# Kernel optimization log

Measured on AMD Instinct MI355X. Metric: run time of the kernel, lower is better.

## Reference

```python
import jax, jax.numpy as jnp
import numpy as np

BS, T_SEG, C, D, N, K, H = 4, 16, 64, 64, 4096, 32, 64
STRIDE = 4
NB, BSZ, NG, BPG = 4, 8, 1, 4  # K = NB*BSZ, NB = NG*BPG (dendritic tree covers all K)
EPS = 1e-8


def _forward(cc_signals, h_prev, prev_messages, trace_prim, trace_key,
             primitives, key_p, decay_logit, dendrite_branch_w, dendrite_group_w,
             fc1_w, fc1_b, fc2_w, fc2_b, mod_lr_logit, conn_indices):
    bs, n, d = h_prev.shape
    # ---- per-neuron modulator MLP: [h, trace_prim, trace_key, primitives, key] -> 3 ----
    mod_input = jnp.concatenate([
        h_prev, trace_prim, trace_key,
        jnp.broadcast_to(primitives[None], (bs, n, d)),
        jnp.broadcast_to(key_p[None], (bs, n, d))], axis=-1)           # [BS,N,5D]
    x = jnp.tanh(jnp.einsum('bnd,ndh->bnh', mod_input, fc1_w) + fc1_b)  # [BS,N,H]
    out3 = jnp.einsum('bnh,nho->bno', x, fc2_w) + fc2_b                 # [BS,N,3]
    gate_prim = jnp.tanh(out3[..., 0:1])
    gate_key = jnp.tanh(out3[..., 1:2])
    decay_mod = out3[..., 2]

    mod_lr = jax.nn.sigmoid(mod_lr_logit)
    tp_dir = trace_prim / jnp.clip(jnp.linalg.norm(trace_prim, axis=-1, keepdims=True), EPS)
    tk_dir = trace_key / jnp.clip(jnp.linalg.norm(trace_key, axis=-1, keepdims=True), EPS)
    eff_prim = primitives[None] + mod_lr * gate_prim * tp_dir           # [BS,N,D]
    eff_key = key_p[None] + mod_lr * gate_key * tk_dir                  # [BS,N,D]
    eff_decay = jax.nn.sigmoid(decay_logit[None] + decay_mod)[..., None]  # [BS,N,1]

    # routing computed once per segment from the initial messages
    routing = jax.nn.sigmoid(
        jnp.einsum('bnd,bnkd->bnk', eff_key, prev_messages[:, conn_indices]))  # [BS,N,K]

    def gather_fc(weighted):  # [BS,N,K,D] -> [BS,N,D] hierarchical dendritic reduce
        tree = weighted.reshape(bs, n, NB, BSZ, d)
        branch = jnp.tanh(jnp.einsum('bnjkd,njkd->bnjd', tree, dendrite_branch_w))  # [BS,N,NB,D]
        grouped = branch.reshape(bs, n, NG, BPG, d)
        group = jnp.tanh(jnp.einsum('bngpd,ngpd->bngd', grouped, dendrite_group_w))  # [BS,N,NG,D]
        return group.mean(axis=2)  # n_tree == K so no leftover term

    cc_steps = jnp.moveaxis(cc_signals[:, ::STRIDE], 0, 1)  # [n_steps,BS,C,D]

    def step(carry, cc_t):
        h, prev_msg = carry
        nm = prev_msg[:, conn_indices]                      # neighbor gather [BS,N,K,D]
        received = gather_fc(routing[..., None] * nm)       # [BS,N,D]
        received = received.at[:, :C].add(cc_t)             # inject port signals
        h = eff_decay * h + (1.0 - eff_decay) * received
        prev_msg = jnp.tanh(h * eff_prim)
        return (h, prev_msg), prev_msg[:, :C]

    (h_final, _), ports = jax.lax.scan(step, (h_prev, prev_messages), cc_steps)
    # each port output is held for `stride` tokens; only the fresh one carries grad
    ports_rep = jnp.repeat(ports, STRIDE, axis=0)            # [T,BS,C,D]
    fresh = (jnp.arange(T_SEG) % STRIDE == 0)[:, None, None, None]
    out = jnp.where(fresh, ports_rep, jax.lax.stop_gradient(ports_rep))
    return jnp.moveaxis(out, 0, 1)                           # [BS,T_seg,C,D]


def setup_inputs() -> dict:
    key = jax.random.key(0)
    ks = jax.random.split(key, 10)

    def rms_init(k, shape):
        raw = jax.random.normal(k, shape, dtype=jnp.float32)
        rms = jnp.clip(jnp.sqrt(jnp.mean(raw ** 2, axis=-1, keepdims=True)), EPS)
        return raw / rms

    cc_signals = jax.random.normal(ks[0], (BS, T_SEG, C, D), dtype=jnp.float32)
    h_prev = 0.1 * jax.random.normal(ks[1], (BS, N, D), dtype=jnp.float32)
    primitives = rms_init(ks[2], (N, D))
    key_p = rms_init(ks[3], (N, D))
    prev_messages = jnp.tanh(h_prev * primitives[None])
    trace_prim = 0.1 * jax.random.normal(ks[4], (BS, N, D), dtype=jnp.float32)
    trace_key = 0.1 * jax.random.normal(ks[5], (BS, N, D), dtype=jnp.float32)
    decay_logit = jnp.zeros((N,), dtype=jnp.float32)
    dendrite_branch_w = jnp.full((N, NB, BSZ, D), 1.0 / BSZ, dtype=jnp.float32)
    dendrite_group_w = jnp.full((N, NG, BPG, D), 1.0 / BPG, dtype=jnp.float32)
    fc1_w = jax.random.normal(ks[6], (N, 5 * D, H), dtype=jnp.float32) * (2.0 / (5 * D + H)) ** 0.5
    fc1_b = jnp.zeros((N, H), dtype=jnp.float32)
    fc2_w = 0.02 * jax.random.normal(ks[7], (N, H, 3), dtype=jnp.float32)
    fc2_b = jnp.zeros((N, 3), dtype=jnp.float32)
    mod_lr_logit = jnp.float32(-2.0)
    conn_indices = jnp.sort(jax.random.randint(ks[8], (N, K), 0, N, dtype=jnp.int32), axis=-1)
    return dict(cc_signals=cc_signals, h_prev=h_prev, prev_messages=prev_messages,
                trace_prim=trace_prim, trace_key=trace_key, primitives=primitives,
                key_p=key_p, decay_logit=decay_logit,
                dendrite_branch_w=dendrite_branch_w, dendrite_group_w=dendrite_group_w,
                fc1_w=fc1_w, fc1_b=fc1_b, fc2_w=fc2_w, fc2_b=fc2_b,
                mod_lr_logit=mod_lr_logit, conn_indices=conn_indices)


def reference(cc_signals, h_prev, prev_messages, trace_prim, trace_key,
              primitives, key_p, decay_logit, dendrite_branch_w, dendrite_group_w,
              fc1_w, fc1_b, fc2_w, fc2_b, mod_lr_logit, conn_indices):
    return _forward(cc_signals, h_prev, prev_messages, trace_prim, trace_key,
                    primitives, key_p, decay_logit, dendrite_branch_w, dendrite_group_w,
                    fc1_w, fc1_b, fc2_w, fc2_b, mod_lr_logit, conn_indices)
```

## Files before the change

kernel.cpp:

```cpp
#include <hip/hip_runtime.h>
#include <math.h>

#define BS 4
#define TSEG 16
#define CC 64
#define DD 64
#define NN 4096
#define KK 32
#define HH 64
#define D5 320

__device__ __forceinline__ float sigm(float x){ return 1.0f/(1.0f+expf(-x)); }

__global__ __launch_bounds__(256) void k_pre(
    const float* __restrict__ h_prev,
    const float* __restrict__ pm0,
    const float* __restrict__ trp,
    const float* __restrict__ trk,
    const float* __restrict__ prim,
    const float* __restrict__ keyp,
    const float* __restrict__ dlog,
    const float* __restrict__ fc1w,
    const float* __restrict__ fc1b,
    const float* __restrict__ fc2w,
    const float* __restrict__ fc2b,
    const float* __restrict__ mll,
    const int*  __restrict__ conn,
    float* __restrict__ ws_h,
    float* __restrict__ ws_ep,
    float* __restrict__ ws_rt,
    float* __restrict__ ws_ed)
{
    __shared__ float mod2[4][D5][4];
    __shared__ int   cn_s[4][KK];
    const int wid  = threadIdx.x >> 6;
    const int lane = threadIdx.x & 63;
    const int n    = (blockIdx.x << 2) + wid;

    #pragma unroll
    for (int b = 0; b < BS; b++) {
        mod2[wid][lane      ][b] = h_prev[((size_t)b*NN + n)*DD + lane];
        mod2[wid][64  + lane][b] = trp  [((size_t)b*NN + n)*DD + lane];
        mod2[wid][128 + lane][b] = trk  [((size_t)b*NN + n)*DD + lane];
    }
    {
        const float pv = prim[(size_t)n*DD + lane];
        const float kv = keyp[(size_t)n*DD + lane];
        #pragma unroll
        for (int b = 0; b < BS; b++) {
            mod2[wid][192 + lane][b] = pv;
            mod2[wid][256 + lane][b] = kv;
        }
    }
    if (lane < KK) cn_s[wid][lane] = conn[(size_t)n*KK + lane];
    __syncthreads();

    float acc[4] = {0.f, 0.f, 0.f, 0.f};
    const float* wp = fc1w + (size_t)n * D5 * HH + lane;
    #pragma unroll 8
    for (int d = 0; d < D5; d++) {
        const float  w  = wp[(size_t)d * HH];
        const float4 mv = *(const float4*)(&mod2[wid][d][0]);
        acc[0] = fmaf(mv.x, w, acc[0]);
        acc[1] = fmaf(mv.y, w, acc[1]);
        acc[2] = fmaf(mv.z, w, acc[2]);
        acc[3] = fmaf(mv.w, w, acc[3]);
    }
    const float b1 = fc1b[(size_t)n*HH + lane];
    float x[4];
    #pragma unroll
    for (int b = 0; b < BS; b++) x[b] = tanhf(acc[b] + b1);

    const float f0 = fc2w[(size_t)n*HH*3 + lane*3 + 0];
    const float f1 = fc2w[(size_t)n*HH*3 + lane*3 + 1];
    const float f2 = fc2w[(size_t)n*HH*3 + lane*3 + 2];
    float po[4][3];
    #pragma unroll
    for (int b = 0; b < BS; b++) { po[b][0]=x[b]*f0; po[b][1]=x[b]*f1; po[b][2]=x[b]*f2; }
    #pragma unroll
    for (int m = 1; m < 64; m <<= 1) {
        #pragma unroll
        for (int b = 0; b < BS; b++) {
            #pragma unroll
            for (int o = 0; o < 3; o++) po[b][o] += __shfl_xor(po[b][o], m, 64);
        }
    }
    const float c0 = fc2b[(size_t)n*3+0];
    const float c1 = fc2b[(size_t)n*3+1];
    const float c2 = fc2b[(size_t)n*3+2];
    const float dl  = dlog[n];
    const float mlr = sigm(mll[0]);
    float gp[4], gk[4], ed[4];
    #pragma unroll
    for (int b = 0; b < BS; b++) {
        gp[b] = tanhf(po[b][0] + c0);
        gk[b] = tanhf(po[b][1] + c1);
        ed[b] = sigm(dl + po[b][2] + c2);
    }
    {
        const float edsel = (lane==0)?ed[0]:(lane==1)?ed[1]:(lane==2)?ed[2]:ed[3];
        if (lane < 4) ws_ed[(size_t)lane*NN + n] = edsel;
    }

    const int d = lane;
    const float4 hpv = *(const float4*)(&mod2[wid][d      ][0]);
    const float4 tpv = *(const float4*)(&mod2[wid][64  + d][0]);
    const float4 tkv = *(const float4*)(&mod2[wid][128 + d][0]);
    const float  pr  = mod2[wid][192 + d][0];
    const float  kp  = mod2[wid][256 + d][0];
    float hp[4] = {hpv.x, hpv.y, hpv.z, hpv.w};
    float tp[4] = {tpv.x, tpv.y, tpv.z, tpv.w};
    float tk[4] = {tkv.x, tkv.y, tkv.z, tkv.w};

    float s2[8];
    #pragma unroll
    for (int b = 0; b < BS; b++) { s2[b] = tp[b]*tp[b]; s2[4+b] = tk[b]*tk[b]; }
    #pragma unroll
    for (int m = 1; m < 64; m <<= 1) {
        #pragma unroll
        for (int i = 0; i < 8; i++) s2[i] += __shfl_xor(s2[i], m, 64);
    }
    float ep[4], ek[4];
    #pragma unroll
    for (int b = 0; b < BS; b++) {
        const float np = fmaxf(sqrtf(s2[b]),   1e-8f);
        const float nk = fmaxf(sqrtf(s2[4+b]), 1e-8f);
        ep[b] = pr + mlr*gp[b]*(tp[b]/np);
        ek[b] = kp + mlr*gk[b]*(tk[b]/nk);
    }
    #pragma unroll
    for (int b = 0; b < BS; b++) {
        ws_ep[((size_t)b*NN + n)*DD + d] = ep[b];
        ws_h [((size_t)b*NN + n)*DD + d] = hp[b];
    }
    #pragma unroll 4
    for (int k = 0; k < KK; k++) {
        const int cn = cn_s[wid][k];
        float rr[4];
        #pragma unroll
        for (int b = 0; b < BS; b++) rr[b] = ek[b]*pm0[((size_t)b*NN + cn)*DD + d];
        #pragma unroll
        for (int m = 1; m < 64; m <<= 1) {
            #pragma unroll
            for (int b = 0; b < BS; b++) rr[b] += __shfl_xor(rr[b], m, 64);
        }
        const float rsel = (lane==0)?rr[0]:(lane==1)?rr[1]:(lane==2)?rr[2]:rr[3];
        if (lane < 4) ws_rt[((size_t)lane*NN + n)*KK + k] = sigm(rsel);
    }
}

__global__ __launch_bounds__(256) void k_step(
    const float* __restrict__ pm_in,
    float* __restrict__ pm_out,
    float* __restrict__ ws_h,
    const float* __restrict__ ws_ep,
    const float* __restrict__ ws_rt,
    const float* __restrict__ ws_ed,
    const float* __restrict__ bw,
    const float* __restrict__ gw,
    const int*  __restrict__ conn,
    const float* __restrict__ cc,
    float* __restrict__ out,
    const int s)
{
    __shared__ float bw_s[2048];
    __shared__ float gw_s[256];
    __shared__ float rt_s[4][KK];
    __shared__ int   cn_s[KK];
    const int n   = blockIdx.x;
    const int tid = threadIdx.x;
    {
        const float4* src = (const float4*)(bw + (size_t)n*2048);
        float4* dst = (float4*)bw_s;
        dst[tid]       = src[tid];
        dst[tid + 256] = src[tid + 256];
        if (tid < 64) ((float4*)gw_s)[tid] = ((const float4*)(gw + (size_t)n*256))[tid];
        if (tid < KK) cn_s[tid] = conn[(size_t)n*KK + tid];
        if (tid < 128) rt_s[tid>>5][tid&31] =
            ws_rt[((size_t)(tid>>5)*NN + n)*KK + (tid & 31)];
    }
    __syncthreads();

    const int b = tid >> 6, d = tid & 63;
    const size_t bn = ((size_t)b*NN + n)*DD + d;

    float bs0=0.f, bs1=0.f, bs2=0.f, bs3=0.f;
    #pragma unroll
    for (int k = 0; k < KK; k++) {
        const int   cn = cn_s[k];
        const float nm = pm_in[((size_t)b*NN + cn)*DD + d];
        const float wg = rt_s[b][k] * nm;
        const float bv = bw_s[k*DD + d];
        if      (k <  8) bs0 = fmaf(wg, bv, bs0);
        else if (k < 16) bs1 = fmaf(wg, bv, bs1);
        else if (k < 24) bs2 = fmaf(wg, bv, bs2);
        else             bs3 = fmaf(wg, bv, bs3);
    }
    const float br0 = tanhf(bs0), br1 = tanhf(bs1), br2 = tanhf(bs2), br3 = tanhf(bs3);
    const float gs = br0*gw_s[d] + br1*gw_s[64+d] + br2*gw_s[128+d] + br3*gw_s[192+d];
    float recv = tanhf(gs);
    if (n < CC) recv += cc[(size_t)((b*TSEG + 4*s)*CC + n)*DD + d];

    const float edv = ws_ed[(size_t)b*NN + n];
    const float hn  = edv*ws_h[bn] + (1.0f - edv)*recv;
    ws_h[bn] = hn;
    const float pmv = tanhf(hn * ws_ep[bn]);
    pm_out[bn] = pmv;
    if (n < CC) {
        #pragma unroll
        for (int r = 0; r < 4; r++)
            out[(size_t)((b*TSEG + 4*s + r)*CC + n)*DD + d] = pmv;
    }
}

extern "C" void kernel_launch(void* const* d_in, const int* in_sizes, int n_in,
                              void* d_out, int out_size, void* d_ws, size_t ws_size,
                              hipStream_t stream) {
    const float* cc    = (const float*)d_in[0];
    const float* h_prev= (const float*)d_in[1];
    const float* pm0   = (const float*)d_in[2];
    const float* trp   = (const float*)d_in[3];
    const float* trk   = (const float*)d_in[4];
    const float* prim  = (const float*)d_in[5];
    const float* keyp  = (const float*)d_in[6];
    const float* dlog  = (const float*)d_in[7];
    const float* bw    = (const float*)d_in[8];
    const float* gw    = (const float*)d_in[9];
    const float* fc1w  = (const float*)d_in[10];
    const float* fc1b  = (const float*)d_in[11];
    const float* fc2w  = (const float*)d_in[12];
    const float* fc2b  = (const float*)d_in[13];
    const float* mll   = (const float*)d_in[14];
    const int*   conn  = (const int*)d_in[15];
    float* out = (float*)d_out;

    float* ws   = (float*)d_ws;
    const size_t BND = (size_t)BS*NN*DD;
    float* ws_h  = ws;
    float* ws_ep = ws + BND;
    float* msgA  = ws + 2*BND;
    float* msgB  = ws + 3*BND;
    float* ws_rt = ws + 4*BND;
    float* ws_ed = ws + 4*BND + (size_t)BS*NN*KK;

    k_pre<<<NN/4, 256, 0, stream>>>(h_prev, pm0, trp, trk, prim, keyp, dlog,
                                    fc1w, fc1b, fc2w, fc2b, mll, conn,
                                    ws_h, ws_ep, ws_rt, ws_ed);

    k_step<<<NN, 256, 0, stream>>>(pm0,  msgA, ws_h, ws_ep, ws_rt, ws_ed,
                                   bw, gw, conn, cc, out, 0);
    k_step<<<NN, 256, 0, stream>>>(msgA, msgB, ws_h, ws_ep, ws_rt, ws_ed,
                                   bw, gw, conn, cc, out, 1);
    k_step<<<NN, 256, 0, stream>>>(msgB, msgA, ws_h, ws_ep, ws_rt, ws_ed,
                                   bw, gw, conn, cc, out, 2);
    k_step<<<NN, 256, 0, stream>>>(msgA, msgB, ws_h, ws_ep, ws_rt, ws_ed,
                                   bw, gw, conn, cc, out, 3);
}
```

Before: 616.8 us.

## Vectorize fc1 and routing in k_pre; make k_step wave-per-neuron with float4 I/O

The fc1 matvec is restructured so each lane loads float4 weight rows and accumulates a 4x4 register tile of batch by hidden outputs. The 320-long input dimension is split across four lane groups, which are then combined with shuffles. The routing dot products and k_step's gather, dendrite and update path now use float4 accesses. k_step maps one wavefront per neuron and four neurons per block, so the block barrier goes away. The initial h copy to the workspace is dropped, and step 0 reads h_prev directly. In exchange there are more live registers and more LDS per block, and the code relies on wavefront-level ordering of LDS writes and reads with no barrier.

```diff
diff --git a/kernel.cpp b/kernel.cpp
--- a/kernel.cpp
+++ b/kernel.cpp
@@ -11,6 +11,9 @@
 #define D5 320
 
 __device__ __forceinline__ float sigm(float x){ return 1.0f/(1.0f+expf(-x)); }
+__device__ __forceinline__ float4 tanh4(float4 v){
+    return make_float4(tanhf(v.x), tanhf(v.y), tanhf(v.z), tanhf(v.w));
+}
 
 __global__ __launch_bounds__(256) void k_pre(
     const float* __restrict__ h_prev,
@@ -26,12 +29,12 @@
     const float* __restrict__ fc2b,
     const float* __restrict__ mll,
     const int*  __restrict__ conn,
-    float* __restrict__ ws_h,
     float* __restrict__ ws_ep,
     float* __restrict__ ws_rt,
     float* __restrict__ ws_ed)
 {
     __shared__ float mod2[4][D5][4];
+    __shared__ float ek_s[4][4][DD];
     __shared__ int   cn_s[4][KK];
     const int wid  = threadIdx.x >> 6;
     const int lane = threadIdx.x & 63;
@@ -53,37 +56,71 @@
         }
     }
     if (lane < KK) cn_s[wid][lane] = conn[(size_t)n*KK + lane];
-    __syncthreads();
-
-    float acc[4] = {0.f, 0.f, 0.f, 0.f};
-    const float* wp = fc1w + (size_t)n * D5 * HH + lane;
-    #pragma unroll 8
-    for (int d = 0; d < D5; d++) {
-        const float  w  = wp[(size_t)d * HH];
-        const float4 mv = *(const float4*)(&mod2[wid][d][0]);
-        acc[0] = fmaf(mv.x, w, acc[0]);
-        acc[1] = fmaf(mv.y, w, acc[1]);
-        acc[2] = fmaf(mv.z, w, acc[2]);
-        acc[3] = fmaf(mv.w, w, acc[3]);
-    }
-    const float b1 = fc1b[(size_t)n*HH + lane];
-    float x[4];
-    #pragma unroll
-    for (int b = 0; b < BS; b++) x[b] = tanhf(acc[b] + b1);
-
-    const float f0 = fc2w[(size_t)n*HH*3 + lane*3 + 0];
-    const float f1 = fc2w[(size_t)n*HH*3 + lane*3 + 1];
-    const float f2 = fc2w[(size_t)n*HH*3 + lane*3 + 2];
-    float po[4][3];
-    #pragma unroll
-    for (int b = 0; b < BS; b++) { po[b][0]=x[b]*f0; po[b][1]=x[b]*f1; po[b][2]=x[b]*f2; }
-    #pragma unroll
-    for (int m = 1; m < 64; m <<= 1) {
-        #pragma unroll
-        for (int b = 0; b < BS; b++) {
-            #pragma unroll
-            for (int o = 0; o < 3; o++) po[b][o] += __shfl_xor(po[b][o], m, 64);
-        }
+
+    const int g  = lane >> 4;
+    const int hq = lane & 15;
+    float acc[16];
+    #pragma unroll
+    for (int i = 0; i < 16; i++) acc[i] = 0.f;
+    const float* wp = fc1w + (size_t)n*D5*HH + (size_t)g*HH + 4*hq;
+    const float* mp = &mod2[wid][g][0];
+    #pragma unroll 4
+    for (int it = 0; it < 80; it++) {
+        const float4 w4 = *(const float4*)(wp + (size_t)it*256);
+        const float4 m4 = *(const float4*)(mp + it*16);
+        acc[ 0] = fmaf(m4.x, w4.x, acc[ 0]);
+        acc[ 1] = fmaf(m4.x, w4.y, acc[ 1]);
+        acc[ 2] = fmaf(m4.x, w4.z, acc[ 2]);
+        acc[ 3] = fmaf(m4.x, w4.w, acc[ 3]);
+        acc[ 4] = fmaf(m4.y, w4.x, acc[ 4]);
+        acc[ 5] = fmaf(m4.y, w4.y, acc[ 5]);
+        acc[ 6] = fmaf(m4.y, w4.z, acc[ 6]);
+        acc[ 7] = fmaf(m4.y, w4.w, acc[ 7]);
+        acc[ 8] = fmaf(m4.z, w4.x, acc[ 8]);
+        acc[ 9] = fmaf(m4.z, w4.y, acc[ 9]);
+        acc[10] = fmaf(m4.z, w4.z, acc[10]);
+        acc[11] = fmaf(m4.z, w4.w, acc[11]);
+        acc[12] = fmaf(m4.w, w4.x, acc[12]);
+        acc[13] = fmaf(m4.w, w4.y, acc[13]);
+        acc[14] = fmaf(m4.w, w4.z, acc[14]);
+        acc[15] = fmaf(m4.w, w4.w, acc[15]);
+    }
+    #pragma unroll
+    for (int i = 0; i < 16; i++) {
+        acc[i] += __shfl_xor(acc[i], 16, 64);
+        acc[i] += __shfl_xor(acc[i], 32, 64);
+    }
+    const float4 b1 = *(const float4*)(fc1b + (size_t)n*HH + 4*hq);
+    float x[16];
+    #pragma unroll
+    for (int b = 0; b < BS; b++) {
+        x[b*4+0] = tanhf(acc[b*4+0] + b1.x);
+        x[b*4+1] = tanhf(acc[b*4+1] + b1.y);
+        x[b*4+2] = tanhf(acc[b*4+2] + b1.z);
+        x[b*4+3] = tanhf(acc[b*4+3] + b1.w);
+    }
+
+    float f2[12];
+    {
+        const float4* f2p = (const float4*)(fc2w + (size_t)n*HH*3 + 12*hq);
+        const float4 fa = f2p[0], fb = f2p[1], fc = f2p[2];
+        f2[0]=fa.x; f2[1]=fa.y; f2[2]=fa.z; f2[3]=fa.w;
+        f2[4]=fb.x; f2[5]=fb.y; f2[6]=fb.z; f2[7]=fb.w;
+        f2[8]=fc.x; f2[9]=fc.y; f2[10]=fc.z; f2[11]=fc.w;
+    }
+    float po[12];
+    #pragma unroll
+    for (int b = 0; b < BS; b++) {
+        #pragma unroll
+        for (int o = 0; o < 3; o++) {
+            po[b*3+o] = x[b*4+0]*f2[0*3+o] + x[b*4+1]*f2[1*3+o]
+                      + x[b*4+2]*f2[2*3+o] + x[b*4+3]*f2[3*3+o];
+        }
+    }
+    #pragma unroll
+    for (int m = 1; m < 16; m <<= 1) {
+        #pragma unroll
+        for (int i = 0; i < 12; i++) po[i] += __shfl_xor(po[i], m, 64);
     }
     const float c0 = fc2b[(size_t)n*3+0];
     const float c1 = fc2b[(size_t)n*3+1];
@@ -93,66 +130,64 @@
     float gp[4], gk[4], ed[4];
     #pragma unroll
     for (int b = 0; b < BS; b++) {
-        gp[b] = tanhf(po[b][0] + c0);
-        gk[b] = tanhf(po[b][1] + c1);
-        ed[b] = sigm(dl + po[b][2] + c2);
-    }
-    {
+        gp[b] = tanhf(po[b*3+0] + c0);
+        gk[b] = tanhf(po[b*3+1] + c1);
+        ed[b] = sigm(dl + po[b*3+2] + c2);
+    }
+    if (lane < 4) {
         const float edsel = (lane==0)?ed[0]:(lane==1)?ed[1]:(lane==2)?ed[2]:ed[3];
-        if (lane < 4) ws_ed[(size_t)lane*NN + n] = edsel;
-    }
-
-    const int d = lane;
-    const float4 hpv = *(const float4*)(&mod2[wid][d      ][0]);
-    const float4 tpv = *(const float4*)(&mod2[wid][64  + d][0]);
-    const float4 tkv = *(const float4*)(&mod2[wid][128 + d][0]);
-    const float  pr  = mod2[wid][192 + d][0];
-    const float  kp  = mod2[wid][256 + d][0];
-    float hp[4] = {hpv.x, hpv.y, hpv.z, hpv.w};
-    float tp[4] = {tpv.x, tpv.y, tpv.z, tpv.w};
-    float tk[4] = {tkv.x, tkv.y, tkv.z, tkv.w};
-
-    float s2[8];
-    #pragma unroll
-    for (int b = 0; b < BS; b++) { s2[b] = tp[b]*tp[b]; s2[4+b] = tk[b]*tk[b]; }
-    #pragma unroll
-    for (int m = 1; m < 64; m <<= 1) {
-        #pragma unroll
-        for (int i = 0; i < 8; i++) s2[i] += __shfl_xor(s2[i], m, 64);
-    }
-    float ep[4], ek[4];
-    #pragma unroll
-    for (int b = 0; b < BS; b++) {
-        const float np = fmaxf(sqrtf(s2[b]),   1e-8f);
-        const float nk = fmaxf(sqrtf(s2[4+b]), 1e-8f);
-        ep[b] = pr + mlr*gp[b]*(tp[b]/np);
-        ek[b] = kp + mlr*gk[b]*(tk[b]/nk);
-    }
-    #pragma unroll
-    for (int b = 0; b < BS; b++) {
-        ws_ep[((size_t)b*NN + n)*DD + d] = ep[b];
-        ws_h [((size_t)b*NN + n)*DD + d] = hp[b];
-    }
-    #pragma unroll 4
-    for (int k = 0; k < KK; k++) {
-        const int cn = cn_s[wid][k];
-        float rr[4];
-        #pragma unroll
-        for (int b = 0; b < BS; b++) rr[b] = ek[b]*pm0[((size_t)b*NN + cn)*DD + d];
+        ws_ed[(size_t)lane*NN + n] = edsel;
+    }
+
+    {
+        const int d = lane;
+        const float4 tpv = *(const float4*)(&mod2[wid][64  + d][0]);
+        const float4 tkv = *(const float4*)(&mod2[wid][128 + d][0]);
+        const float  pr  = mod2[wid][192 + d][0];
+        const float  kp  = mod2[wid][256 + d][0];
+        float tp[4] = {tpv.x, tpv.y, tpv.z, tpv.w};
+        float tk[4] = {tkv.x, tkv.y, tkv.z, tkv.w};
+        float s2[8];
+        #pragma unroll
+        for (int b = 0; b < BS; b++) { s2[b] = tp[b]*tp[b]; s2[4+b] = tk[b]*tk[b]; }
         #pragma unroll
         for (int m = 1; m < 64; m <<= 1) {
             #pragma unroll
-            for (int b = 0; b < BS; b++) rr[b] += __shfl_xor(rr[b], m, 64);
-        }
-        const float rsel = (lane==0)?rr[0]:(lane==1)?rr[1]:(lane==2)?rr[2]:rr[3];
-        if (lane < 4) ws_rt[((size_t)lane*NN + n)*KK + k] = sigm(rsel);
+            for (int i = 0; i < 8; i++) s2[i] += __shfl_xor(s2[i], m, 64);
+        }
+        #pragma unroll
+        for (int b = 0; b < BS; b++) {
+            const float np = fmaxf(sqrtf(s2[b]),   1e-8f);
+            const float nk = fmaxf(sqrtf(s2[4+b]), 1e-8f);
+            const float ep = pr + mlr*gp[b]*(tp[b]/np);
+            const float ek = kp + mlr*gk[b]*(tk[b]/nk);
+            ws_ep[((size_t)b*NN + n)*DD + d] = ep;
+            ek_s[wid][b][d] = ek;
+        }
+    }
+
+    {
+        const int bb = lane >> 4, dq = lane & 15;
+        const float4 ekq = *(const float4*)(&ek_s[wid][bb][4*dq]);
+        #pragma unroll 8
+        for (int k = 0; k < KK; k++) {
+            const int cn = cn_s[wid][k];
+            const float4 pm4 = *(const float4*)(pm0 + ((size_t)bb*NN + cn)*DD + 4*dq);
+            float rr = ekq.x*pm4.x + ekq.y*pm4.y + ekq.z*pm4.z + ekq.w*pm4.w;
+            rr += __shfl_xor(rr, 1, 64);
+            rr += __shfl_xor(rr, 2, 64);
+            rr += __shfl_xor(rr, 4, 64);
+            rr += __shfl_xor(rr, 8, 64);
+            if (dq == 0) ws_rt[((size_t)bb*NN + n)*KK + k] = sigm(rr);
+        }
     }
 }
 
 __global__ __launch_bounds__(256) void k_step(
     const float* __restrict__ pm_in,
     float* __restrict__ pm_out,
-    float* __restrict__ ws_h,
+    const float* __restrict__ h_in,
+    float* __restrict__ h_out,
     const float* __restrict__ ws_ep,
     const float* __restrict__ ws_rt,
     const float* __restrict__ ws_ed,
@@ -163,53 +198,75 @@
     float* __restrict__ out,
     const int s)
 {
-    __shared__ float bw_s[2048];
-    __shared__ float gw_s[256];
-    __shared__ float rt_s[4][KK];
-    __shared__ int   cn_s[KK];
-    const int n   = blockIdx.x;
-    const int tid = threadIdx.x;
+    __shared__ float bw_s[4][2048];
+    __shared__ float gw_s[4][256];
+    __shared__ float rt_s[4][4][KK];
+    __shared__ int   cn_s[4][KK];
+    const int wid  = threadIdx.x >> 6;
+    const int lane = threadIdx.x & 63;
+    const int n    = (blockIdx.x << 2) + wid;
+
     {
         const float4* src = (const float4*)(bw + (size_t)n*2048);
-        float4* dst = (float4*)bw_s;
-        dst[tid]       = src[tid];
-        dst[tid + 256] = src[tid + 256];
-        if (tid < 64) ((float4*)gw_s)[tid] = ((const float4*)(gw + (size_t)n*256))[tid];
-        if (tid < KK) cn_s[tid] = conn[(size_t)n*KK + tid];
-        if (tid < 128) rt_s[tid>>5][tid&31] =
-            ws_rt[((size_t)(tid>>5)*NN + n)*KK + (tid & 31)];
-    }
-    __syncthreads();
-
-    const int b = tid >> 6, d = tid & 63;
-    const size_t bn = ((size_t)b*NN + n)*DD + d;
-
-    float bs0=0.f, bs1=0.f, bs2=0.f, bs3=0.f;
+        float4* dst = (float4*)bw_s[wid];
+        #pragma unroll
+        for (int i = 0; i < 8; i++) dst[i*64 + lane] = src[i*64 + lane];
+        ((float4*)gw_s[wid])[lane] = ((const float4*)(gw + (size_t)n*256))[lane];
+        rt_s[wid][lane>>5][lane&31] =
+            ws_rt[((size_t)(lane>>5)*NN + n)*KK + (lane&31)];
+        rt_s[wid][2+(lane>>5)][lane&31] =
+            ws_rt[((size_t)(2+(lane>>5))*NN + n)*KK + (lane&31)];
+        if (lane < KK) cn_s[wid][lane] = conn[(size_t)n*KK + lane];
+    }
+
+    const int b = lane >> 4, dq = lane & 15;
+    const int d0 = 4*dq;
+    const size_t bnd = ((size_t)b*NN + n)*DD + d0;
+
+    float4 bs[4];
+    #pragma unroll
+    for (int j = 0; j < 4; j++) bs[j] = make_float4(0.f,0.f,0.f,0.f);
     #pragma unroll
     for (int k = 0; k < KK; k++) {
-        const int   cn = cn_s[k];
-        const float nm = pm_in[((size_t)b*NN + cn)*DD + d];
-        const float wg = rt_s[b][k] * nm;
-        const float bv = bw_s[k*DD + d];
-        if      (k <  8) bs0 = fmaf(wg, bv, bs0);
-        else if (k < 16) bs1 = fmaf(wg, bv, bs1);
-        else if (k < 24) bs2 = fmaf(wg, bv, bs2);
-        else             bs3 = fmaf(wg, bv, bs3);
-    }
-    const float br0 = tanhf(bs0), br1 = tanhf(bs1), br2 = tanhf(bs2), br3 = tanhf(bs3);
-    const float gs = br0*gw_s[d] + br1*gw_s[64+d] + br2*gw_s[128+d] + br3*gw_s[192+d];
-    float recv = tanhf(gs);
-    if (n < CC) recv += cc[(size_t)((b*TSEG + 4*s)*CC + n)*DD + d];
-
+        const int cn = cn_s[wid][k];
+        const float4 nm = *(const float4*)(pm_in + ((size_t)b*NN + cn)*DD + d0);
+        const float  w  = rt_s[wid][b][k];
+        const float4 bv = *(const float4*)(&bw_s[wid][k*DD + d0]);
+        const int j = k >> 3;
+        bs[j].x = fmaf(w*nm.x, bv.x, bs[j].x);
+        bs[j].y = fmaf(w*nm.y, bv.y, bs[j].y);
+        bs[j].z = fmaf(w*nm.z, bv.z, bs[j].z);
+        bs[j].w = fmaf(w*nm.w, bv.w, bs[j].w);
+    }
+    float4 gs = make_float4(0.f,0.f,0.f,0.f);
+    #pragma unroll
+    for (int j = 0; j < 4; j++) {
+        const float4 br = tanh4(bs[j]);
+        const float4 gv = *(const float4*)(&gw_s[wid][j*DD + d0]);
+        gs.x = fmaf(br.x, gv.x, gs.x);
+        gs.y = fmaf(br.y, gv.y, gs.y);
+        gs.z = fmaf(br.z, gv.z, gs.z);
+        gs.w = fmaf(br.w, gv.w, gs.w);
+    }
+    float4 recv = tanh4(gs);
+    if (n < CC) {
+        const float4 cv = *(const float4*)(cc + (size_t)((b*TSEG + 4*s)*CC + n)*DD + d0);
+        recv.x += cv.x; recv.y += cv.y; recv.z += cv.z; recv.w += cv.w;
+    }
     const float edv = ws_ed[(size_t)b*NN + n];
-    const float hn  = edv*ws_h[bn] + (1.0f - edv)*recv;
-    ws_h[bn] = hn;
-    const float pmv = tanhf(hn * ws_ep[bn]);
-    pm_out[bn] = pmv;
+    float4 h = *(const float4*)(h_in + bnd);
+    h.x = edv*h.x + (1.f-edv)*recv.x;
+    h.y = edv*h.y + (1.f-edv)*recv.y;
+    h.z = edv*h.z + (1.f-edv)*recv.z;
+    h.w = edv*h.w + (1.f-edv)*recv.w;
+    *(float4*)(h_out + bnd) = h;
+    const float4 ep = *(const float4*)(ws_ep + bnd);
+    const float4 pm = tanh4(make_float4(h.x*ep.x, h.y*ep.y, h.z*ep.z, h.w*ep.w));
+    *(float4*)(pm_out + bnd) = pm;
     if (n < CC) {
         #pragma unroll
         for (int r = 0; r < 4; r++)
-            out[(size_t)((b*TSEG + 4*s + r)*CC + n)*DD + d] = pmv;
+            *(float4*)(out + (size_t)((b*TSEG + 4*s + r)*CC + n)*DD + d0) = pm;
     }
 }
 
@@ -245,14 +302,14 @@
 
     k_pre<<<NN/4, 256, 0, stream>>>(h_prev, pm0, trp, trk, prim, keyp, dlog,
                                     fc1w, fc1b, fc2w, fc2b, mll, conn,
-                                    ws_h, ws_ep, ws_rt, ws_ed);
-
-    k_step<<<NN, 256, 0, stream>>>(pm0,  msgA, ws_h, ws_ep, ws_rt, ws_ed,
-                                   bw, gw, conn, cc, out, 0);
-    k_step<<<NN, 256, 0, stream>>>(msgA, msgB, ws_h, ws_ep, ws_rt, ws_ed,
-                                   bw, gw, conn, cc, out, 1);
-    k_step<<<NN, 256, 0, stream>>>(msgB, msgA, ws_h, ws_ep, ws_rt, ws_ed,
-                                   bw, gw, conn, cc, out, 2);
-    k_step<<<NN, 256, 0, stream>>>(msgA, msgB, ws_h, ws_ep, ws_rt, ws_ed,
-                                   bw, gw, conn, cc, out, 3);
+                                    ws_ep, ws_rt, ws_ed);
+
+    k_step<<<NN/4, 256, 0, stream>>>(pm0,  msgA, h_prev, ws_h, ws_ep, ws_rt, ws_ed,
+                                     bw, gw, conn, cc, out, 0);
+    k_step<<<NN/4, 256, 0, stream>>>(msgA, msgB, ws_h, ws_h, ws_ep, ws_rt, ws_ed,
+                                     bw, gw, conn, cc, out, 1);
+    k_step<<<NN/4, 256, 0, stream>>>(msgB, msgA, ws_h, ws_h, ws_ep, ws_rt, ws_ed,
+                                     bw, gw, conn, cc, out, 2);
+    k_step<<<NN/4, 256, 0, stream>>>(msgA, msgB, ws_h, ws_h, ws_ep, ws_rt, ws_ed,
+                                     bw, gw, conn, cc, out, 3);
 }
```

New measurement: 618.1 us. No clear change (+0.2%).
